# Performance work log

Measured on AMD Instinct MI355X. Metric: run time of the kernel, lower is better.

The kernel has to match this reference:

```python
import jax, jax.numpy as jnp
import numpy as np

F = 16384   # n_features
D = 768     # d_model
B = 2       # batch
S = 256     # seq len
C = 16      # connections per downstream feature
M = F * C   # total connections


def setup_inputs() -> dict:
    key = jax.random.key(0)
    k1, k2, k3, k4 = jax.random.split(key, 4)
    up_facts = jax.random.normal(k1, (B, S, F), dtype=jnp.float32)
    down_encoder = jax.random.normal(k2, (F, D), dtype=jnp.float32) * 0.02
    up_decoder = jax.random.normal(k3, (D, F), dtype=jnp.float32) * 0.02
    # connection_mask.nonzero() is row-major: i sorted, C targets per row
    i_indices = jnp.repeat(jnp.arange(F, dtype=jnp.int32), C)  # [M]
    j_indices = jax.random.randint(k4, (M,), 0, F, dtype=jnp.int32)  # [M]
    return {
        "up_facts": up_facts,
        "down_encoder": down_encoder,
        "up_decoder": up_decoder,
        "i_indices": i_indices,
        "j_indices": j_indices,
    }


def reference(up_facts, down_encoder, up_decoder, i_indices, j_indices):
    # up_facts: [B,S,F]; down_encoder: [F,D]; up_decoder: [D,F]
    b, s, f = up_facts.shape
    m = i_indices.shape[0]
    # per-connection virtual weight: values[m] = down_encoder[i[m]] . up_decoder[:, j[m]]
    values = jnp.einsum("md,dm->m", down_encoder[i_indices], up_decoder[:, j_indices])  # [M]
    # gather upstream feature activations and scale
    scaled = up_facts[:, :, j_indices] * values[None, None, :]  # [B,S,M]
    # scatter_add over last axis into downstream feature bins (i is constant across B,S)
    flat = scaled.reshape(b * s, m).T  # [M, B*S]
    contrib = jax.ops.segment_sum(flat, i_indices, num_segments=f)  # [F, B*S]
    return contrib.T.reshape(b, s, f)
```

## Files before the change

### kernel.cpp

```cpp
#include <hip/hip_runtime.h>
#include <hip/hip_bf16.h>

#define F_ 16384
#define D_ 768
#define C_ 16
#define BS_ 512
#define M_ (F_*C_)

static __device__ __forceinline__ float bf2f(unsigned short u) {
    return __uint_as_float(((unsigned int)u) << 16);
}
static __device__ __forceinline__ unsigned short f2bf(float f) {
    return __bfloat16_as_ushort(__float2bfloat16(f));
}

#if __has_builtin(__builtin_amdgcn_sdot4)
static __device__ __forceinline__ int sdot4(unsigned int a, unsigned int b, int c) {
    return __builtin_amdgcn_sdot4((int)a, (int)b, c, false);
}
#else
static __device__ __forceinline__ int sdot4(unsigned int a, unsigned int b, int c) {
#pragma unroll
    for (int i = 0; i < 4; ++i)
        c += (int)(signed char)(a >> (8 * i)) * (int)(signed char)(b >> (8 * i));
    return c;
}
#endif

__global__ __launch_bounds__(256) void k_transpose_i8(const float* __restrict__ in,
                                                      unsigned char* __restrict__ out,
                                                      float* __restrict__ scales) {
    __shared__ float tile[64][65];
    __shared__ float pmax[4][64];
    int c4 = threadIdx.x & 15;
    int r  = threadIdx.x >> 4;
    int fbase = blockIdx.x * 64;
    int dbase = blockIdx.y * 64;
#pragma unroll
    for (int k = 0; k < 4; ++k) {
        int drow = r + k * 16;
        float4 v = *(const float4*)(in + (size_t)(dbase + drow) * F_ + fbase + c4 * 4);
        tile[drow][c4 * 4 + 0] = v.x;
        tile[drow][c4 * 4 + 1] = v.y;
        tile[drow][c4 * 4 + 2] = v.z;
        tile[drow][c4 * 4 + 3] = v.w;
    }
    __syncthreads();
    {
        int c = threadIdx.x & 63;
        int q = threadIdx.x >> 6;
        float m = 0.f;
#pragma unroll
        for (int i = 0; i < 16; ++i)
            m = fmaxf(m, fabsf(tile[q * 16 + i][c]));
        pmax[q][c] = m;
    }
    __syncthreads();
    int dp = threadIdx.x & 15;
    int fr = threadIdx.x >> 4;
#pragma unroll
    for (int k = 0; k < 4; ++k) {
        int frow = fr + k * 16;
        float cmax = fmaxf(fmaxf(pmax[0][frow], pmax[1][frow]),
                           fmaxf(pmax[2][frow], pmax[3][frow]));
        float s  = cmax * (1.f / 127.f);
        float rs = cmax > 0.f ? 127.f / cmax : 0.f;
        int q0 = __float2int_rn(tile[4 * dp + 0][frow] * rs);
        int q1 = __float2int_rn(tile[4 * dp + 1][frow] * rs);
        int q2 = __float2int_rn(tile[4 * dp + 2][frow] * rs);
        int q3 = __float2int_rn(tile[4 * dp + 3][frow] * rs);
        unsigned int p = (q0 & 0xff) | ((q1 & 0xff) << 8)
                       | ((q2 & 0xff) << 16) | ((q3 & 0xff) << 24);
        *(unsigned int*)(out + (size_t)(fbase + frow) * D_ + dbase + dp * 4) = p;
        if (dp == 0)
            scales[((size_t)(fbase + frow) << 4) + (dbase >> 6)] = s;
    }
}

__global__ __launch_bounds__(256) void k_values(const float* __restrict__ enc,
                                                const unsigned char* __restrict__ dec8,
                                                const float* __restrict__ scales,
                                                const int* __restrict__ jidx,
                                                unsigned int* __restrict__ packed) {
    int f = blockIdx.x;
    int lane = threadIdx.x & 63;
    int wave = threadIdx.x >> 6;
    const float4* erow = (const float4*)(enc + (size_t)f * D_);
    float4 e[3];
    e[0] = erow[lane];
    e[1] = erow[lane + 64];
    e[2] = erow[lane + 128];
    int4 j4 = *(const int4*)(jidx + (f << 4) + (wave << 2));
    int js[4] = {j4.x, j4.y, j4.z, j4.w};
    unsigned int g[4][3];
    float sd[4][3];
    int sb = lane >> 4;
#pragma unroll
    for (int t = 0; t < 4; ++t) {
        const unsigned int* drow = (const unsigned int*)(dec8 + (size_t)js[t] * D_);
        g[t][0] = drow[lane];
        g[t][1] = drow[lane + 64];
        g[t][2] = drow[lane + 128];
        const float* srow = scales + ((size_t)js[t] << 4);
        sd[t][0] = srow[sb];
        sd[t][1] = srow[sb + 4];
        sd[t][2] = srow[sb + 8];
    }
    unsigned int eq[3];
    float se[3];
#pragma unroll
    for (int k = 0; k < 3; ++k) {
        float4 v = e[k];
        float m = fmaxf(fmaxf(fabsf(v.x), fabsf(v.y)),
                        fmaxf(fabsf(v.z), fabsf(v.w)));
#pragma unroll
        for (int off = 1; off < 16; off <<= 1)
            m = fmaxf(m, __shfl_xor(m, off, 64));
        float rs = m > 0.f ? 127.f / m : 0.f;
        se[k] = m * (1.f / 127.f);
        int q0 = __float2int_rn(v.x * rs);
        int q1 = __float2int_rn(v.y * rs);
        int q2 = __float2int_rn(v.z * rs);
        int q3 = __float2int_rn(v.w * rs);
        eq[k] = (q0 & 0xff) | ((q1 & 0xff) << 8)
              | ((q2 & 0xff) << 16) | ((q3 & 0xff) << 24);
    }
#pragma unroll
    for (int t = 0; t < 4; ++t) {
        float acc = 0.f;
#pragma unroll
        for (int k = 0; k < 3; ++k) {
            int d = sdot4(eq[k], g[t][k], 0);
            acc = fmaf((float)d, se[k] * sd[t][k], acc);
        }
#pragma unroll
        for (int off = 32; off > 0; off >>= 1)
            acc += __shfl_down(acc, off, 64);
        if (lane == 0)
            packed[(f << 4) + (wave << 2) + t] =
                ((unsigned int)f2bf(acc) << 16) | (unsigned int)js[t];
    }
}

__global__ __launch_bounds__(512) void k_out(const float* __restrict__ up,
                                             const unsigned int* __restrict__ packed,
                                             float* __restrict__ out) {
    __shared__ unsigned int rowp[F_];
    int bs0  = (blockIdx.x >> 1) << 1;
    int half = blockIdx.x & 1;
    const float4* u0 = (const float4*)(up + (size_t)bs0 * F_);
    const float4* u1 = (const float4*)(up + (size_t)(bs0 + 1) * F_);
#pragma unroll
    for (int k = 0; k < 8; ++k) {
        int idx = threadIdx.x + k * 512;
        float4 a = u0[idx];
        float4 b = u1[idx];
        uint4 p;
        p.x = ((unsigned int)f2bf(b.x) << 16) | (unsigned int)f2bf(a.x);
        p.y = ((unsigned int)f2bf(b.y) << 16) | (unsigned int)f2bf(a.y);
        p.z = ((unsigned int)f2bf(b.z) << 16) | (unsigned int)f2bf(a.z);
        p.w = ((unsigned int)f2bf(b.w) << 16) | (unsigned int)f2bf(a.w);
        ((uint4*)rowp)[idx] = p;
    }
    __syncthreads();
    int f0 = half << 13;
#pragma unroll 4
    for (int it = 0; it < 16; ++it) {
        int f = f0 + threadIdx.x + it * 512;
        const uint4* sp = (const uint4*)(packed + ((size_t)f << 4));
        float a0 = 0.f, a1 = 0.f;
#pragma unroll
        for (int q = 0; q < 4; ++q) {
            uint4 w = sp[q];
#define CONN(ww) { unsigned int p_ = rowp[(ww) & 0xffffu];                  \
                   float v_ = __uint_as_float((ww) & 0xffff0000u);          \
                   a0 += __uint_as_float(p_ << 16) * v_;                    \
                   a1 += __uint_as_float(p_ & 0xffff0000u) * v_; }
            CONN(w.x) CONN(w.y) CONN(w.z) CONN(w.w)
#undef CONN
        }
        out[(size_t)bs0 * F_ + f] = a0;
        out[(size_t)(bs0 + 1) * F_ + f] = a1;
    }
}

extern "C" void kernel_launch(void* const* d_in, const int* in_sizes, int n_in,
                              void* d_out, int out_size, void* d_ws, size_t ws_size,
                              hipStream_t stream) {
    const float* up   = (const float*)d_in[0];
    const float* enc  = (const float*)d_in[1];
    const float* dec  = (const float*)d_in[2];
    const int*   jidx = (const int*)d_in[4];
    float*       out  = (float*)d_out;

    size_t dec8_bytes  = (size_t)F_ * D_;
    size_t scale_bytes = (size_t)F_ * 16 * sizeof(float);
    unsigned char* dec8   = (unsigned char*)d_ws;
    float*         scales = (float*)((char*)d_ws + dec8_bytes);
    unsigned int*  packed = (unsigned int*)((char*)d_ws + dec8_bytes + scale_bytes);

    k_transpose_i8<<<dim3(F_ / 64, D_ / 64), 256, 0, stream>>>(dec, dec8, scales);
    k_values<<<F_, 256, 0, stream>>>(enc, dec8, scales, jidx, packed);
    k_out<<<BS_, 512, 0, stream>>>(up, packed, out);
}
```

Before: 205.8 us.

## Restructure values kernel to 8 lanes per connection; give each k_out block full feature range

The values kernel now handles two downstream features per block. Even waves quantize the encoder row into LDS, then 8 lanes cooperate on each connection, using 16-byte loads of the int8 decoder row and chained sdot4 with a short shuffle reduction. Before, a whole wave reduced each connection with 4-byte loads. k_out now launches one block per row pair covering all features instead of two half blocks, so the bf16 up_facts LDS tile is built once per pair rather than twice. The trade-off is fewer blocks in k_out (256) on a large GPU, and a sync plus idle odd waves during quantization in k_values.

```diff
diff --git a/kernel.cpp b/kernel.cpp
--- a/kernel.cpp
+++ b/kernel.cpp
@@ -26,6 +26,15 @@
     return c;
 }
 #endif
+
+static __device__ __forceinline__ int chain8(uint4 ea, uint4 eb, uint4 ga, uint4 gb) {
+    int a = 0;
+    a = sdot4(ea.x, ga.x, a); a = sdot4(ea.y, ga.y, a);
+    a = sdot4(ea.z, ga.z, a); a = sdot4(ea.w, ga.w, a);
+    a = sdot4(eb.x, gb.x, a); a = sdot4(eb.y, gb.y, a);
+    a = sdot4(eb.z, gb.z, a); a = sdot4(eb.w, gb.w, a);
+    return a;
+}
 
 __global__ __launch_bounds__(256) void k_transpose_i8(const float* __restrict__ in,
                                                       unsigned char* __restrict__ out,
@@ -82,72 +91,72 @@
                                                 const float* __restrict__ scales,
                                                 const int* __restrict__ jidx,
                                                 unsigned int* __restrict__ packed) {
-    int f = blockIdx.x;
+    __shared__ __align__(16) unsigned int enc8_lds[2][192];
+    __shared__ float se_lds[2][12];
     int lane = threadIdx.x & 63;
     int wave = threadIdx.x >> 6;
-    const float4* erow = (const float4*)(enc + (size_t)f * D_);
-    float4 e[3];
-    e[0] = erow[lane];
-    e[1] = erow[lane + 64];
-    e[2] = erow[lane + 128];
-    int4 j4 = *(const int4*)(jidx + (f << 4) + (wave << 2));
-    int js[4] = {j4.x, j4.y, j4.z, j4.w};
-    unsigned int g[4][3];
-    float sd[4][3];
-    int sb = lane >> 4;
-#pragma unroll
-    for (int t = 0; t < 4; ++t) {
-        const unsigned int* drow = (const unsigned int*)(dec8 + (size_t)js[t] * D_);
-        g[t][0] = drow[lane];
-        g[t][1] = drow[lane + 64];
-        g[t][2] = drow[lane + 128];
-        const float* srow = scales + ((size_t)js[t] << 4);
-        sd[t][0] = srow[sb];
-        sd[t][1] = srow[sb + 4];
-        sd[t][2] = srow[sb + 8];
-    }
-    unsigned int eq[3];
-    float se[3];
-#pragma unroll
-    for (int k = 0; k < 3; ++k) {
-        float4 v = e[k];
-        float m = fmaxf(fmaxf(fabsf(v.x), fabsf(v.y)),
-                        fmaxf(fabsf(v.z), fabsf(v.w)));
-#pragma unroll
-        for (int off = 1; off < 16; off <<= 1)
-            m = fmaxf(m, __shfl_xor(m, off, 64));
-        float rs = m > 0.f ? 127.f / m : 0.f;
-        se[k] = m * (1.f / 127.f);
-        int q0 = __float2int_rn(v.x * rs);
-        int q1 = __float2int_rn(v.y * rs);
-        int q2 = __float2int_rn(v.z * rs);
-        int q3 = __float2int_rn(v.w * rs);
-        eq[k] = (q0 & 0xff) | ((q1 & 0xff) << 8)
-              | ((q2 & 0xff) << 16) | ((q3 & 0xff) << 24);
-    }
-#pragma unroll
-    for (int t = 0; t < 4; ++t) {
-        float acc = 0.f;
+    int fl   = wave >> 1;
+    int f    = (blockIdx.x << 1) + fl;
+
+    if ((wave & 1) == 0) {
+        const float4* erow = (const float4*)(enc + (size_t)f * D_);
+        float4 e0 = erow[lane], e1 = erow[lane + 64], e2 = erow[lane + 128];
+        float4 ev[3] = {e0, e1, e2};
 #pragma unroll
         for (int k = 0; k < 3; ++k) {
-            int d = sdot4(eq[k], g[t][k], 0);
-            acc = fmaf((float)d, se[k] * sd[t][k], acc);
+            float4 v = ev[k];
+            float m = fmaxf(fmaxf(fabsf(v.x), fabsf(v.y)),
+                            fmaxf(fabsf(v.z), fabsf(v.w)));
+#pragma unroll
+            for (int off = 1; off < 16; off <<= 1)
+                m = fmaxf(m, __shfl_xor(m, off, 64));
+            float rs = m > 0.f ? 127.f / m : 0.f;
+            int q0 = __float2int_rn(v.x * rs);
+            int q1 = __float2int_rn(v.y * rs);
+            int q2 = __float2int_rn(v.z * rs);
+            int q3 = __float2int_rn(v.w * rs);
+            enc8_lds[fl][lane + 64 * k] = (q0 & 0xff) | ((q1 & 0xff) << 8)
+                                        | ((q2 & 0xff) << 16) | ((q3 & 0xff) << 24);
+            if ((lane & 15) == 0)
+                se_lds[fl][4 * k + (lane >> 4)] = m * (1.f / 127.f);
         }
-#pragma unroll
-        for (int off = 32; off > 0; off >>= 1)
-            acc += __shfl_down(acc, off, 64);
-        if (lane == 0)
-            packed[(f << 4) + (wave << 2) + t] =
-                ((unsigned int)f2bf(acc) << 16) | (unsigned int)js[t];
-    }
+    }
+    __syncthreads();
+
+    int t = ((wave & 1) << 3) + (lane >> 3);
+    int p = lane & 7;
+    int j = jidx[(f << 4) + t];
+
+    const uint4* grow = (const uint4*)(dec8 + (size_t)j * D_);
+    uint4 g0 = grow[6 * p + 0], g1 = grow[6 * p + 1], g2 = grow[6 * p + 2],
+          g3 = grow[6 * p + 3], g4 = grow[6 * p + 4], g5 = grow[6 * p + 5];
+    const uint4* elds = (const uint4*)enc8_lds[fl];
+    uint4 e0 = elds[6 * p + 0], e1 = elds[6 * p + 1], e2 = elds[6 * p + 2],
+          e3 = elds[6 * p + 3], e4 = elds[6 * p + 4], e5 = elds[6 * p + 5];
+
+    int b0 = (3 * p) >> 1, b1 = (3 * p + 1) >> 1, b2 = (3 * p + 2) >> 1;
+    const float* srow = scales + ((size_t)j << 4);
+    float s0 = srow[b0] * se_lds[fl][b0];
+    float s1 = srow[b1] * se_lds[fl][b1];
+    float s2 = srow[b2] * se_lds[fl][b2];
+
+    int a0 = chain8(e0, e1, g0, g1);
+    int a1 = chain8(e2, e3, g2, g3);
+    int a2 = chain8(e4, e5, g4, g5);
+    float val = fmaf((float)a0, s0, fmaf((float)a1, s1, (float)a2 * s2));
+
+#pragma unroll
+    for (int off = 1; off < 8; off <<= 1)
+        val += __shfl_down(val, off, 64);
+    if (p == 0)
+        packed[(f << 4) + t] = ((unsigned int)f2bf(val) << 16) | (unsigned int)j;
 }
 
 __global__ __launch_bounds__(512) void k_out(const float* __restrict__ up,
                                              const unsigned int* __restrict__ packed,
                                              float* __restrict__ out) {
     __shared__ unsigned int rowp[F_];
-    int bs0  = (blockIdx.x >> 1) << 1;
-    int half = blockIdx.x & 1;
+    int bs0 = blockIdx.x << 1;
     const float4* u0 = (const float4*)(up + (size_t)bs0 * F_);
     const float4* u1 = (const float4*)(up + (size_t)(bs0 + 1) * F_);
 #pragma unroll
@@ -163,10 +172,9 @@
         ((uint4*)rowp)[idx] = p;
     }
     __syncthreads();
-    int f0 = half << 13;
 #pragma unroll 4
-    for (int it = 0; it < 16; ++it) {
-        int f = f0 + threadIdx.x + it * 512;
+    for (int it = 0; it < 32; ++it) {
+        int f = threadIdx.x + it * 512;
         const uint4* sp = (const uint4*)(packed + ((size_t)f << 4));
         float a0 = 0.f, a1 = 0.f;
 #pragma unroll
@@ -200,6 +208,6 @@
     unsigned int*  packed = (unsigned int*)((char*)d_ws + dec8_bytes + scale_bytes);
 
     k_transpose_i8<<<dim3(F_ / 64, D_ / 64), 256, 0, stream>>>(dec, dec8, scales);
-    k_values<<<F_, 256, 0, stream>>>(enc, dec8, scales, jidx, packed);
-    k_out<<<BS_, 512, 0, stream>>>(up, packed, out);
-}
+    k_values<<<F_ / 2, 256, 0, stream>>>(enc, dec8, scales, jidx, packed);
+    k_out<<<BS_ / 2, 512, 0, stream>>>(up, packed, out);
+}
```

Measured after the change: 215.6 us. +4.8%, slower.
